# Kernel tuning notes

Measured on AMD Instinct MI355X. Metric: run time of the kernel, lower is better.

Reference implementation:

```python
import jax, jax.numpy as jnp
import numpy as np


def setup_inputs() -> dict:
    key = jax.random.key(0)
    ks = jax.random.split(key, 9)
    B, S, D, DK, DV = 4, 4096, 1024, 128, 128
    scale = 1.0 / np.sqrt(D)
    return {
        "q": jax.random.normal(ks[0], (B, S, D), jnp.float32),
        "k": jax.random.normal(ks[1], (B, S, D), jnp.float32),
        "v": jax.random.normal(ks[2], (B, S, D), jnp.float32),
        "Wq": jax.random.normal(ks[3], (D, DK), jnp.float32) * scale,
        "bq": jnp.zeros((DK,), jnp.float32),
        "Wk": jax.random.normal(ks[4], (D, DK), jnp.float32) * scale,
        "bk": jnp.zeros((DK,), jnp.float32),
        "Wv": jax.random.normal(ks[5], (D, DV), jnp.float32) * scale,
        "bv": jnp.zeros((DV,), jnp.float32),
    }


def reference(q, k, v, Wq, bq, Wk, bk, Wv, bv):
    # Q/K/V projections (nn.Linear)
    Q = q @ Wq + bq          # [B,S,DK]
    K = k @ Wk + bk          # [B,S,DK]
    V = v @ Wv + bv          # [B,S,DV]
    scale = Q.shape[-1] ** 0.5
    scores = jnp.einsum("bqd,bkd->bqk", Q, K) / scale  # [B,Sq,Sk]
    attn = jax.nn.softmax(scores, axis=-1)
    return jnp.einsum("bqk,bkd->bqd", attn, V)          # [B,Sq,DV]
```

## Files before the change

### kernel.cpp

```cpp
#include <hip/hip_runtime.h>
#include <hip/hip_bf16.h>
#include <cstdint>
#include <cmath>


typedef __bf16 bf16x8 __attribute__((ext_vector_type(8)));
typedef float f32x4 __attribute__((ext_vector_type(4)));
typedef float f32x16 __attribute__((ext_vector_type(16)));

typedef const __attribute__((address_space(1))) unsigned int* gp_t;
typedef __attribute__((address_space(3))) unsigned int* lp_t;

__device__ __forceinline__ unsigned short f2bf(float f) {
  unsigned u = __float_as_uint(f);
  u += 0x7fffu + ((u >> 16) & 1u);
  return (unsigned short)(u >> 16);
}

__device__ __forceinline__ bf16x8 ld_frag(const char* p) {
  uint4 u = *reinterpret_cast<const uint4*>(p);
  return __builtin_bit_cast(bf16x8, u);
}

__device__ __forceinline__ unsigned cvtpk_bf16(float lo, float hi) {
  unsigned r;
  asm("v_cvt_pk_bf16_f32 %0, %1, %2" : "=v"(r) : "v"(lo), "v"(hi));
  return r;
}

__device__ __forceinline__ void pl32swap(unsigned &a, unsigned &b) {
  asm("v_permlane32_swap_b32 %0, %1" : "+v"(a), "+v"(b));
}

__device__ __forceinline__ bf16x8 mk_frag(unsigned w0, unsigned w1, unsigned w2, unsigned w3) {
  uint4 u{w0, w1, w2, w3};
  return __builtin_bit_cast(bf16x8, u);
}

__device__ __forceinline__ bf16x8 cvt_frag(const float4& f0, const float4& f1) {
  return mk_frag(cvtpk_bf16(f0.x, f0.y), cvtpk_bf16(f0.z, f0.w),
                 cvtpk_bf16(f1.x, f1.y), cvtpk_bf16(f1.z, f1.w));
}

#define QSCALE_LOG2E 0.12751744f

__global__ __launch_bounds__(256) void prep_wt_kernel(
    const float* __restrict__ W0, const float* __restrict__ W1, const float* __restrict__ W2,
    unsigned short* __restrict__ T0, unsigned short* __restrict__ T1,
    unsigned short* __restrict__ T2) {
  const int mode = blockIdx.z;
  const float* W = (mode == 0) ? W0 : (mode == 1) ? W1 : W2;
  unsigned short* Wt = (mode == 0) ? T0 : (mode == 1) ? T1 : T2;
  __shared__ float tile[64][65];
  int kt = blockIdx.x, nt = blockIdx.y;
  int tid = threadIdx.x;
  int c = tid & 63;
  int r0 = (tid >> 6) * 16;
#pragma unroll
  for (int i = 0; i < 16; ++i) {
    int r = r0 + i;
    tile[r][c] = W[(size_t)(kt * 64 + r) * 128 + nt * 64 + c];
  }
  __syncthreads();
#pragma unroll
  for (int i = 0; i < 16; ++i) {
    int n = r0 + i;
    Wt[(size_t)(nt * 64 + n) * 1024 + kt * 64 + c] = f2bf(tile[c][n]);
  }
}

__global__ __launch_bounds__(512, 4) void proj_kernel(
    const float* __restrict__ qx, const float* __restrict__ kx, const float* __restrict__ vx,
    const unsigned short* __restrict__ Wtq, const unsigned short* __restrict__ Wtk,
    const unsigned short* __restrict__ Wtv,
    const float* __restrict__ bq, const float* __restrict__ bk, const float* __restrict__ bv,
    unsigned short* __restrict__ Qb, unsigned short* __restrict__ Kb,
    unsigned short* __restrict__ Vtb) {
  const int mode = blockIdx.y;
  const float* x = (mode == 0) ? qx : (mode == 1) ? kx : vx;
  const unsigned short* Wt = (mode == 0) ? Wtq : (mode == 1) ? Wtk : Wtv;
  const float* bias = (mode == 0) ? bq : (mode == 1) ? bk : bv;

  __shared__ __align__(16) char ldsW[49152];

  const int tid = threadIdx.x;
  const int lane = tid & 63, wid = tid >> 6;
  const int l15 = lane & 15, hi = lane >> 4;
  const long row0 = (long)blockIdx.x * 128;

  const float* a_base = x + (row0 + wid * 16 + l15) * 1024 + hi * 8;

  const char* w_src = (const char*)Wt + (size_t)(tid >> 3) * 2048 +
                      (size_t)((tid & 7) ^ ((tid >> 3) & 7)) * 16;

  f32x4 acc[8];
#pragma unroll
  for (int i = 0; i < 8; ++i) acc[i] = f32x4{0.f, 0.f, 0.f, 0.f};

  float4 aA[4], aB[4];

#define PROJ_STAGE_W(TS)                                                              \
  {                                                                                   \
    char* lw_ = ldsW + ((TS) % 3) * 16384;                                            \
    _Pragma("unroll")                                                                 \
    for (int i = 0; i < 2; ++i)                                                       \
      __builtin_amdgcn_global_load_lds((gp_t)(w_src + (size_t)i * 131072 + (TS) * 128),\
                                       (lp_t)(lw_ + i * 8192 + wid * 1024), 16, 0, 0);\
  }

#pragma unroll
  for (int kk = 0; kk < 2; ++kk)
#pragma unroll
    for (int h = 0; h < 2; ++h)
      aA[kk * 2 + h] = *reinterpret_cast<const float4*>(a_base + kk * 32 + h * 4);
  PROJ_STAGE_W(0);
  PROJ_STAGE_W(1);

#define PROJ_ITER(T, CUR, NXT)                                                        \
  {                                                                                   \
    if ((T) < 15) asm volatile("s_waitcnt vmcnt(2)" ::: "memory");                    \
    else          asm volatile("s_waitcnt vmcnt(0)" ::: "memory");                    \
    __builtin_amdgcn_s_barrier();                                                     \
    __builtin_amdgcn_sched_barrier(0);                                                \
    if ((T) < 15) {                                                                   \
      _Pragma("unroll")                                                               \
      for (int kk = 0; kk < 2; ++kk)                                                  \
        _Pragma("unroll")                                                             \
        for (int h = 0; h < 2; ++h)                                                   \
          NXT[kk * 2 + h] = *reinterpret_cast<const float4*>(                         \
              a_base + ((T) + 1) * 64 + kk * 32 + h * 4);                             \
    }                                                                                 \
    if ((T) < 14) PROJ_STAGE_W((T) + 2);                                              \
    bf16x8 af0 = cvt_frag(CUR[0], CUR[1]);                                            \
    bf16x8 af1 = cvt_frag(CUR[2], CUR[3]);                                            \
    char* lwc_ = ldsW + ((T) % 3) * 16384;                                            \
    __builtin_amdgcn_s_setprio(1);                                                    \
    _Pragma("unroll")                                                                 \
    for (int ni = 0; ni < 8; ++ni) {                                                  \
      int row = ni * 16 + l15;                                                        \
      int swz = (row & 7) << 4;                                                       \
      bf16x8 wf0 = ld_frag(lwc_ + ((row * 128 + hi * 16) ^ swz));                     \
      bf16x8 wf1 = ld_frag(lwc_ + ((row * 128 + 64 + hi * 16) ^ swz));                \
      acc[ni] = __builtin_amdgcn_mfma_f32_16x16x32_bf16(af0, wf0, acc[ni], 0, 0, 0);  \
      acc[ni] = __builtin_amdgcn_mfma_f32_16x16x32_bf16(af1, wf1, acc[ni], 0, 0, 0);  \
    }                                                                                 \
    __builtin_amdgcn_s_setprio(0);                                                    \
  }

#pragma unroll
  for (int t = 0; t < 16; ++t) {
    if (t & 1) PROJ_ITER(t, aB, aA)
    else       PROJ_ITER(t, aA, aB)
  }

#undef PROJ_ITER
#undef PROJ_STAGE_W

#pragma unroll
  for (int ni = 0; ni < 8; ++ni) {
    int n = ni * 16 + l15;
    float bv_ = bias[n];
    long m = row0 + wid * 16 + hi * 4;
    f32x4 a = acc[ni];
    if (mode == 2) {
      int bb = (int)(m >> 12);
      int s = (int)(m & 4095);
      ushort4 pk;
      pk.x = f2bf(a.x + bv_); pk.y = f2bf(a.y + bv_);
      pk.z = f2bf(a.z + bv_); pk.w = f2bf(a.w + bv_);
      *reinterpret_cast<ushort4*>(Vtb + ((size_t)(bb * 128 + n)) * 4096 + s) = pk;
    } else {
      const float sc = (mode == 0) ? QSCALE_LOG2E : 1.0f;
      unsigned short* outp = (mode == 0) ? Qb : Kb;
      outp[(m + 0) * 128 + n] = f2bf((a.x + bv_) * sc);
      outp[(m + 1) * 128 + n] = f2bf((a.y + bv_) * sc);
      outp[(m + 2) * 128 + n] = f2bf((a.z + bv_) * sc);
      outp[(m + 3) * 128 + n] = f2bf((a.w + bv_) * sc);
    }
  }
}

__global__ __launch_bounds__(256, 2) void attn_kernel(
    const unsigned short* __restrict__ Qb, const unsigned short* __restrict__ Kb,
    const unsigned short* __restrict__ Vtb, float* __restrict__ Po,
    float* __restrict__ ml, int tps) {
  __shared__ uint4 ldsK4[1024];
  __shared__ uint4 ldsV4[1024];
  char* ldsK = (char*)ldsK4;
  char* ldsV = (char*)ldsV4;

  const int tid = threadIdx.x;
  const int lane = tid & 63, wid = tid >> 6;
  const int l31 = lane & 31, hi = lane >> 5;
  const int split = blockIdx.y;
  const int b = blockIdx.z;
  const int qbase = blockIdx.x * 128 + wid * 32;
  const size_t growq = (size_t)b * 4096 + qbase + l31;

  bf16x8 qf[8];
  {
    const unsigned short* qp = Qb + growq * 128 + hi * 8;
#pragma unroll
    for (int kt = 0; kt < 8; ++kt)
      qf[kt] = __builtin_bit_cast(bf16x8, *reinterpret_cast<const uint4*>(qp + kt * 16));
  }

  f32x16 oacc[4];
#pragma unroll
  for (int d = 0; d < 4; ++d)
#pragma unroll
    for (int j = 0; j < 16; ++j) oacc[d][j] = 0.f;
  float mrun = -INFINITY, lrun = 0.f;

  const int t0 = split * tps, t1 = t0 + tps;

  for (int t = t0; t < t1; ++t) {
    const int kv0 = t * 64;
    const char* kg = (const char*)Kb + ((size_t)(b * 4096) + kv0) * 256;
#pragma unroll
    for (int i = 0; i < 4; ++i) {
      int u = tid + 256 * i;
      int row = u >> 4, c = u & 15;
      uint4 val = *reinterpret_cast<const uint4*>(kg + row * 256 + c * 16);
      *reinterpret_cast<uint4*>(ldsK + ((row * 256 + c * 16) ^ ((row & 7) << 4))) = val;
    }
    const char* vg = (const char*)Vtb + (size_t)b * 128 * 4096 * 2 + (size_t)kv0 * 2;
#pragma unroll
    for (int i = 0; i < 4; ++i) {
      int u = tid + 256 * i;
      int dv = u >> 3, c = u & 7;
      uint4 val = *reinterpret_cast<const uint4*>(vg + (size_t)dv * 8192 + c * 16);
      *reinterpret_cast<uint4*>(ldsV + ((dv * 128 + c * 16) ^ ((dv & 7) << 4))) = val;
    }
    __syncthreads();

    f32x16 sc0, sc1;
#pragma unroll
    for (int j = 0; j < 16; ++j) { sc0[j] = 0.f; sc1[j] = 0.f; }
    __builtin_amdgcn_s_setprio(1);
#pragma unroll
    for (int kvb = 0; kvb < 2; ++kvb) {
      int row = kvb * 32 + l31;
      int rowoff = row * 256, swz = (row & 7) << 4;
#pragma unroll
      for (int kt = 0; kt < 8; ++kt) {
        bf16x8 kf = ld_frag(ldsK + ((rowoff + kt * 32 + hi * 16) ^ swz));
        if (kvb == 0) sc0 = __builtin_amdgcn_mfma_f32_32x32x16_bf16(kf, qf[kt], sc0, 0, 0, 0);
        else          sc1 = __builtin_amdgcn_mfma_f32_32x32x16_bf16(kf, qf[kt], sc1, 0, 0, 0);
      }
    }
    __builtin_amdgcn_s_setprio(0);

    float tmx[16];
#pragma unroll
    for (int i = 0; i < 16; ++i) tmx[i] = fmaxf(sc0[i], sc1[i]);
#pragma unroll
    for (int s = 8; s > 0; s >>= 1)
#pragma unroll
      for (int i = 0; i < s; ++i) tmx[i] = fmaxf(tmx[i], tmx[i + s]);
    float mt = tmx[0];
    mt = fmaxf(mt, __shfl_xor(mt, 32));

    if (!__all(mt - mrun <= 8.0f)) {
      float mnew = fmaxf(mrun, mt);
      float scl = exp2f(mrun - mnew);
      mrun = mnew;
      lrun *= scl;
#pragma unroll
      for (int d = 0; d < 4; ++d)
#pragma unroll
        for (int j = 0; j < 16; ++j) oacc[d][j] *= scl;
    }

#pragma unroll
    for (int i = 0; i < 16; ++i) {
      sc0[i] = exp2f(sc0[i] - mrun);
      sc1[i] = exp2f(sc1[i] - mrun);
    }
    float ts[16];
#pragma unroll
    for (int i = 0; i < 16; ++i) ts[i] = sc0[i] + sc1[i];
#pragma unroll
    for (int s = 8; s > 0; s >>= 1)
#pragma unroll
      for (int i = 0; i < s; ++i) ts[i] += ts[i + s];
    float psum = ts[0];
    psum += __shfl_xor(psum, 32);
    lrun += psum;

    bf16x8 pa[4];
#pragma unroll
    for (int c = 0; c < 2; ++c) {
      const f32x16& p = c ? sc1 : sc0;
#pragma unroll
      for (int g = 0; g < 2; ++g) {
        const int base = g * 8;
        unsigned a0 = cvtpk_bf16(p[base + 0], p[base + 1]);
        unsigned b0 = cvtpk_bf16(p[base + 4], p[base + 5]);
        pl32swap(a0, b0);
        unsigned a1 = cvtpk_bf16(p[base + 2], p[base + 3]);
        unsigned b1 = cvtpk_bf16(p[base + 6], p[base + 7]);
        pl32swap(a1, b1);
        pa[c * 2 + g] = mk_frag(a0, a1, b0, b1);
      }
    }

    __builtin_amdgcn_s_setprio(1);
#pragma unroll
    for (int dvb = 0; dvb < 4; ++dvb) {
      int vrow = dvb * 32 + l31;
      int voff = vrow * 128, vswz = (vrow & 7) << 4;
#pragma unroll
      for (int tt = 0; tt < 4; ++tt) {
        bf16x8 vf = ld_frag(ldsV + ((voff + tt * 32 + hi * 16) ^ vswz));
        oacc[dvb] = __builtin_amdgcn_mfma_f32_32x32x16_bf16(vf, pa[tt], oacc[dvb], 0, 0, 0);
      }
    }
    __builtin_amdgcn_s_setprio(0);
    __syncthreads();
  }

  if (hi == 0) {
    float* mlp = ml + (size_t)split * 32768 + growq * 2;
    mlp[0] = mrun; mlp[1] = lrun;
  }

  float* po = Po + ((size_t)split << 21) + ((size_t)b * 4096 + qbase) * 128;
  char* tbase = ldsK + wid * 4096;
  for (int dvb = 0; dvb < 4; ++dvb) {
#pragma unroll
    for (int g = 0; g < 4; ++g) {
      float4 w4{oacc[dvb][g * 4 + 0], oacc[dvb][g * 4 + 1],
                oacc[dvb][g * 4 + 2], oacc[dvb][g * 4 + 3]};
      int off = (l31 * 128 + g * 32 + hi * 16) ^ ((l31 & 7) << 4);
      *reinterpret_cast<float4*>(tbase + off) = w4;
    }
    asm volatile("s_waitcnt lgkmcnt(0)" ::: "memory");
    __builtin_amdgcn_sched_barrier(0);
#pragma unroll
    for (int qq = 0; qq < 4; ++qq) {
      int q = qq * 8 + (lane >> 3);
      int off = (q * 128 + (lane & 7) * 16) ^ ((q & 7) << 4);
      float4 r4 = *reinterpret_cast<const float4*>(tbase + off);
      *reinterpret_cast<float4*>(po + (size_t)q * 128 + dvb * 32 + (lane & 7) * 4) = r4;
    }
    asm volatile("s_waitcnt lgkmcnt(0)" ::: "memory");
    __builtin_amdgcn_sched_barrier(0);
  }
}

template <int NS>
__global__ __launch_bounds__(256) void combine_kernel(const float* __restrict__ Po,
                                                      const float* __restrict__ ml,
                                                      float* __restrict__ out) {
  int idx = blockIdx.x * 256 + threadIdx.x;
  int grow = idx >> 5;
  int c4 = (idx & 31) * 4;
  float m[NS], l[NS];
  float M = -INFINITY;
#pragma unroll
  for (int s = 0; s < NS; ++s) {
    m[s] = ml[(size_t)s * 32768 + grow * 2 + 0];
    l[s] = ml[(size_t)s * 32768 + grow * 2 + 1];
    M = fmaxf(M, m[s]);
  }
  float L = 0.f, w[NS];
#pragma unroll
  for (int s = 0; s < NS; ++s) {
    w[s] = exp2f(m[s] - M);
    L += l[s] * w[s];
  }
  float invL = 1.0f / L;
  float4 acc = {0.f, 0.f, 0.f, 0.f};
#pragma unroll
  for (int s = 0; s < NS; ++s) {
    float4 p = *reinterpret_cast<const float4*>(Po + ((size_t)s << 21) + (size_t)grow * 128 + c4);
    acc.x += p.x * w[s]; acc.y += p.y * w[s];
    acc.z += p.z * w[s]; acc.w += p.w * w[s];
  }
  acc.x *= invL; acc.y *= invL; acc.z *= invL; acc.w *= invL;
  *reinterpret_cast<float4*>(out + (size_t)grow * 128 + c4) = acc;
}

extern "C" void kernel_launch(void* const* d_in, const int* in_sizes, int n_in,
                              void* d_out, int out_size, void* d_ws, size_t ws_size,
                              hipStream_t stream) {
  const float* q  = (const float*)d_in[0];
  const float* k  = (const float*)d_in[1];
  const float* v  = (const float*)d_in[2];
  const float* Wq = (const float*)d_in[3];
  const float* bq = (const float*)d_in[4];
  const float* Wk = (const float*)d_in[5];
  const float* bk = (const float*)d_in[6];
  const float* Wv = (const float*)d_in[7];
  const float* bv = (const float*)d_in[8];
  float* out = (float*)d_out;

  char* ws = (char*)d_ws;
  unsigned short* Qb  = (unsigned short*)(ws);
  unsigned short* Kb  = (unsigned short*)(ws + (4u << 20));
  unsigned short* Vtb = (unsigned short*)(ws + (8u << 20));
  unsigned short* Wtq = (unsigned short*)(ws + (12u << 20));
  unsigned short* Wtk = (unsigned short*)(ws + (12u << 20) + (256u << 10));
  unsigned short* Wtv = (unsigned short*)(ws + (12u << 20) + (512u << 10));

  const size_t base = (size_t)13 << 20;
  const size_t per = ((size_t)8 << 20) + ((size_t)128 << 10);
  int nsplit = 1;
  if (ws_size >= base + 4 * per) nsplit = 4;
  else if (ws_size >= base + 2 * per) nsplit = 2;
  float* Po = (float*)(ws + base);
  float* ml = (float*)(ws + base + (size_t)nsplit * ((size_t)8 << 20));

  prep_wt_kernel<<<dim3(16, 2, 3), 256, 0, stream>>>(Wq, Wk, Wv, Wtq, Wtk, Wtv);
  proj_kernel<<<dim3(128, 3), 512, 0, stream>>>(q, k, v, Wtq, Wtk, Wtv, bq, bk, bv, Qb, Kb, Vtb);
  attn_kernel<<<dim3(32, nsplit, 4), 256, 0, stream>>>(Qb, Kb, Vtb, Po, ml, 64 / nsplit);
  if (nsplit == 4)      combine_kernel<4><<<2048, 256, 0, stream>>>(Po, ml, out);
  else if (nsplit == 2) combine_kernel<2><<<2048, 256, 0, stream>>>(Po, ml, out);
  else                  combine_kernel<1><<<2048, 256, 0, stream>>>(Po, ml, out);
}
```

Before: 105.2 us.

## Double-buffer K/V tiles in attention via async global_load_lds prefetch

The attention kernel now stages K and V tiles straight from global memory into LDS with global_load_lds, using two buffers. The next-but-one tile is prefetched while the current tile is computed, with vmcnt waits and raw barriers in place of __syncthreads. This hides global load latency behind the MFMA work and drops the register round-trip through VGPRs. In exchange LDS use doubles to 64KB per block, which may cut occupancy below the launch-bound target of 2 blocks per CU. The tile count per split also becomes a template parameter.

```diff
diff --git a/kernel.cpp b/kernel.cpp
--- a/kernel.cpp
+++ b/kernel.cpp
@@ -89,7 +89,6 @@
   const long row0 = (long)blockIdx.x * 128;
 
   const float* a_base = x + (row0 + wid * 16 + l15) * 1024 + hi * 8;
-
   const char* w_src = (const char*)Wt + (size_t)(tid >> 3) * 2048 +
                       (size_t)((tid & 7) ^ ((tid >> 3) & 7)) * 16;
 
@@ -180,14 +179,12 @@
   }
 }
 
+template <int TPS>
 __global__ __launch_bounds__(256, 2) void attn_kernel(
     const unsigned short* __restrict__ Qb, const unsigned short* __restrict__ Kb,
     const unsigned short* __restrict__ Vtb, float* __restrict__ Po,
-    float* __restrict__ ml, int tps) {
-  __shared__ uint4 ldsK4[1024];
-  __shared__ uint4 ldsV4[1024];
-  char* ldsK = (char*)ldsK4;
-  char* ldsV = (char*)ldsV4;
+    float* __restrict__ ml) {
+  __shared__ __align__(16) char lds[65536];
 
   const int tid = threadIdx.x;
   const int lane = tid & 63, wid = tid >> 6;
@@ -197,6 +194,29 @@
   const int qbase = blockIdx.x * 128 + wid * 32;
   const size_t growq = (size_t)b * 4096 + qbase + l31;
 
+  const char* kg0 = (const char*)Kb + (size_t)(b * 4096) * 256;
+  const char* vg0 = (const char*)Vtb + (size_t)b * 128 * 4096 * 2;
+  const int k_row = tid >> 4;
+  const int k_csw = (tid & 15) ^ (k_row & 7);
+  const int v_dv = tid >> 3;
+  const int v_csw = (tid & 7) ^ (v_dv & 7);
+
+#define ATTN_STAGE(KV0, BUF)                                                          \
+  {                                                                                   \
+    char* kb_ = lds + (BUF) * 16384;                                                  \
+    char* vb_ = lds + 32768 + (BUF) * 16384;                                          \
+    const char* kgs_ = kg0 + (size_t)(KV0) * 256 + (size_t)k_row * 256 + k_csw * 16;  \
+    const char* vgs_ = vg0 + (size_t)(KV0) * 2 + (size_t)v_dv * 8192 + v_csw * 16;    \
+    _Pragma("unroll")                                                                 \
+    for (int i = 0; i < 4; ++i)                                                       \
+      __builtin_amdgcn_global_load_lds((gp_t)(kgs_ + (size_t)i * 4096),               \
+                                       (lp_t)(kb_ + i * 4096 + wid * 1024), 16, 0, 0);\
+    _Pragma("unroll")                                                                 \
+    for (int i = 0; i < 4; ++i)                                                       \
+      __builtin_amdgcn_global_load_lds((gp_t)(vgs_ + (size_t)i * 262144),             \
+                                       (lp_t)(vb_ + i * 4096 + wid * 1024), 16, 0, 0);\
+  }
+
   bf16x8 qf[8];
   {
     const unsigned short* qp = Qb + growq * 128 + hi * 8;
@@ -212,27 +232,20 @@
     for (int j = 0; j < 16; ++j) oacc[d][j] = 0.f;
   float mrun = -INFINITY, lrun = 0.f;
 
-  const int t0 = split * tps, t1 = t0 + tps;
-
+  const int t0 = split * TPS, t1 = t0 + TPS;
+
+  ATTN_STAGE(t0 * 64, 0);
+  ATTN_STAGE((t0 + 1) * 64, 1);
+
+#pragma unroll 1
   for (int t = t0; t < t1; ++t) {
-    const int kv0 = t * 64;
-    const char* kg = (const char*)Kb + ((size_t)(b * 4096) + kv0) * 256;
-#pragma unroll
-    for (int i = 0; i < 4; ++i) {
-      int u = tid + 256 * i;
-      int row = u >> 4, c = u & 15;
-      uint4 val = *reinterpret_cast<const uint4*>(kg + row * 256 + c * 16);
-      *reinterpret_cast<uint4*>(ldsK + ((row * 256 + c * 16) ^ ((row & 7) << 4))) = val;
-    }
-    const char* vg = (const char*)Vtb + (size_t)b * 128 * 4096 * 2 + (size_t)kv0 * 2;
-#pragma unroll
-    for (int i = 0; i < 4; ++i) {
-      int u = tid + 256 * i;
-      int dv = u >> 3, c = u & 7;
-      uint4 val = *reinterpret_cast<const uint4*>(vg + (size_t)dv * 8192 + c * 16);
-      *reinterpret_cast<uint4*>(ldsV + ((dv * 128 + c * 16) ^ ((dv & 7) << 4))) = val;
-    }
-    __syncthreads();
+    const int buf = (t - t0) & 1;
+    if (t < t1 - 1) asm volatile("s_waitcnt vmcnt(8)" ::: "memory");
+    else            asm volatile("s_waitcnt vmcnt(0)" ::: "memory");
+    __builtin_amdgcn_s_barrier();
+    __builtin_amdgcn_sched_barrier(0);
+    char* ldsK = lds + buf * 16384;
+    char* ldsV = lds + 32768 + buf * 16384;
 
     f32x16 sc0, sc1;
 #pragma unroll
@@ -317,8 +330,13 @@
       }
     }
     __builtin_amdgcn_s_setprio(0);
-    __syncthreads();
-  }
+
+    __builtin_amdgcn_s_barrier();
+    __builtin_amdgcn_sched_barrier(0);
+    if (t + 2 < t1) ATTN_STAGE((t + 2) * 64, buf);
+  }
+
+#undef ATTN_STAGE
 
   if (hi == 0) {
     float* mlp = ml + (size_t)split * 32768 + growq * 2;
@@ -326,7 +344,7 @@
   }
 
   float* po = Po + ((size_t)split << 21) + ((size_t)b * 4096 + qbase) * 128;
-  char* tbase = ldsK + wid * 4096;
+  char* tbase = lds + wid * 4096;
   for (int dvb = 0; dvb < 4; ++dvb) {
 #pragma unroll
     for (int g = 0; g < 4; ++g) {
@@ -414,8 +432,14 @@
 
   prep_wt_kernel<<<dim3(16, 2, 3), 256, 0, stream>>>(Wq, Wk, Wv, Wtq, Wtk, Wtv);
   proj_kernel<<<dim3(128, 3), 512, 0, stream>>>(q, k, v, Wtq, Wtk, Wtv, bq, bk, bv, Qb, Kb, Vtb);
-  attn_kernel<<<dim3(32, nsplit, 4), 256, 0, stream>>>(Qb, Kb, Vtb, Po, ml, 64 / nsplit);
-  if (nsplit == 4)      combine_kernel<4><<<2048, 256, 0, stream>>>(Po, ml, out);
-  else if (nsplit == 2) combine_kernel<2><<<2048, 256, 0, stream>>>(Po, ml, out);
-  else                  combine_kernel<1><<<2048, 256, 0, stream>>>(Po, ml, out);
-}
+  if (nsplit == 4) {
+    attn_kernel<16><<<dim3(32, 4, 4), 256, 0, stream>>>(Qb, Kb, Vtb, Po, ml);
+    combine_kernel<4><<<2048, 256, 0, stream>>>(Po, ml, out);
+  } else if (nsplit == 2) {
+    attn_kernel<32><<<dim3(32, 2, 4), 256, 0, stream>>>(Qb, Kb, Vtb, Po, ml);
+    combine_kernel<2><<<2048, 256, 0, stream>>>(Po, ml, out);
+  } else {
+    attn_kernel<64><<<dim3(32, 1, 4), 256, 0, stream>>>(Qb, Kb, Vtb, Po, ml);
+    combine_kernel<1><<<2048, 256, 0, stream>>>(Po, ml, out);
+  }
+}
```

Measured after the change: 103.6 us. No clear change (-1.5%).
